# Performance work log

Hardware: AMD Instinct MI355X
Metric: run time of the kernel (lower is better)

The kernel has to match this reference:

```python
import jax, jax.numpy as jnp
import numpy as np

# Constants derived from init_kwargs (nuScenes occupancy setup)
XYZ_MIN = jnp.array([-40.0, -40.0, -1.0], dtype=jnp.float32)
XYZ_MAX = jnp.array([40.0, 40.0, 5.4], dtype=jnp.float32)
STEPSIZE = 0.5
_ext = np.array([80.0, 80.0, 6.4])
VOXEL_SIZE = float((_ext.prod() / (200 * 200 * 16)) ** (1.0 / 3.0))  # = 0.4
N_SAMPLES = int(np.linalg.norm(np.array([100, 100, 8]) + 1) / STEPSIZE) + 1  # 287


def trilinear_sample(grid, pts):
    """grid: (C, Dx, Dy, Dz) laid out as [C, x, y, z]; pts: (M, 3) world xyz -> (M, C).
    Matches torch F.grid_sample(align_corners=True) after the coord flip in grid_sampler:
    normalized coord u in [0,1] maps to index u*(dim-1)."""
    C, Dx, Dy, Dz = grid.shape
    dims = jnp.array([Dx, Dy, Dz], dtype=pts.dtype)
    u = (pts - XYZ_MIN) / (XYZ_MAX - XYZ_MIN)
    idx = jnp.clip(u * (dims - 1.0), 0.0, dims - 1.0)  # out-of-bbox pts are masked later
    i0 = jnp.clip(jnp.floor(idx), 0.0, dims - 2.0).astype(jnp.int32)
    w = idx - i0  # (M, 3) in [0, 1]
    flat = grid.reshape(C, -1)
    out = jnp.zeros((C, pts.shape[0]), dtype=pts.dtype)
    for ox in (0, 1):
        wx = w[:, 0] if ox else 1.0 - w[:, 0]
        for oy in (0, 1):
            wy = w[:, 1] if oy else 1.0 - w[:, 1]
            for oz in (0, 1):
                wz = w[:, 2] if oz else 1.0 - w[:, 2]
                lin = ((i0[:, 0] + ox) * Dy + (i0[:, 1] + oy)) * Dz + (i0[:, 2] + oz)
                out = out + jnp.take(flat, lin, axis=1) * (wx * wy * wz)
    return out.T


def _forward(rays_o, rays_d, voxel, rgb_recon):
    ro = rays_o.reshape(-1, 3)
    rd = rays_d.reshape(-1, 3)
    R = ro.shape[0]
    # test-mode sampling: rng = arange(N_samples), Zval = stepsize * voxel_size * rng
    zval = (STEPSIZE * VOXEL_SIZE) * jnp.arange(N_SAMPLES, dtype=ro.dtype)  # (N,)
    pts = ro[:, None, :] + rd[:, None, :] * zval[None, :, None]  # (R, N, 3)
    inside = jnp.all((pts >= XYZ_MIN) & (pts <= XYZ_MAX), axis=-1)  # ~mask_outbbox, (R, N)
    flat_pts = pts.reshape(-1, 3)
    # density sigmoid -> 'prob' compositing
    dens = trilinear_sample(voxel, flat_pts).reshape(R, N_SAMPLES)
    sig = jax.nn.sigmoid(dens)
    # probs = 0 outside bbox; last sample forced to 1 unless inside (then overwritten by sig)
    probs = jnp.where(inside, sig, 0.0)
    probs = probs.at[:, -1].set(jnp.where(inside[:, -1], sig[:, -1], 1.0))
    cum = jnp.minimum(jnp.cumsum(probs, axis=1), 1.0)  # cumsum.clamp(max=1)
    probs = jnp.diff(cum, axis=1, prepend=jnp.zeros((R, 1), cum.dtype))
    depth = jnp.sum(probs * zval[None, :], axis=-1)  # (R,)
    # rgb rendering (img_recon_head=True)
    rgb = trilinear_sample(rgb_recon, flat_pts).reshape(R, N_SAMPLES, 3)
    rgb = jnp.where(inside[..., None], rgb, 0.0)
    rgb_marched = jnp.sum(probs[..., None] * rgb, axis=-2)  # (R, 3)
    return depth, rgb_marched


def setup_inputs() -> dict:
    key = jax.random.key(0)
    k1, k2, k3, k4 = jax.random.split(key, 4)
    num_cam, H, W = 6, 90, 160
    # camera origins near the scene center, inside the bbox
    rays_o = (jax.random.uniform(k1, (num_cam, H, W, 3), jnp.float32) - 0.5) \
        * jnp.array([4.0, 4.0, 1.0], jnp.float32) + jnp.array([0.0, 0.0, 1.5], jnp.float32)
    d = jax.random.normal(k2, (num_cam, H, W, 3), jnp.float32)
    rays_d = d / jnp.linalg.norm(d, axis=-1, keepdims=True)
    voxel = jax.random.normal(k3, (1, 200, 200, 16), jnp.float32)
    rgb_recon = jax.random.uniform(k4, (3, 200, 200, 16), jnp.float32)
    return {"rays_o": rays_o, "rays_d": rays_d, "voxel": voxel, "rgb_recon": rgb_recon}


def reference(rays_o, rays_d, voxel, rgb_recon):
    return _forward(rays_o, rays_d, voxel, rgb_recon)
```

## Files before the change

kernel.cpp:

```cpp
#include <hip/hip_runtime.h>
#include <hip/hip_bf16.h>


namespace {
constexpr int DX = 200, DY = 200, DZ = 16;
constexpr int GRID_N = DX * DY * DZ;
constexpr int NS = 287;
constexpr float ZSTEP = 0.2f;
}

extern "C" __global__ void __launch_bounds__(256)
nerf_march_kernel(const float* __restrict__ ro,
                  const float* __restrict__ rd,
                  const float* __restrict__ vox,
                  const float* __restrict__ rgbg,
                  float* __restrict__ out, int R)
{
    const int r = blockIdx.x * blockDim.x + threadIdx.x;
    if (r >= R) return;

    const float ox = ro[3 * r + 0];
    const float oy = ro[3 * r + 1];
    const float oz = ro[3 * r + 2];
    const float dx = rd[3 * r + 0];
    const float dy = rd[3 * r + 1];
    const float dz = rd[3 * r + 2];

    float c = 0.0f;
    float depth = 0.0f;
    float a0 = 0.0f, a1 = 0.0f, a2 = 0.0f;
    const float zlast = ZSTEP * (float)(NS - 1);

    #pragma unroll 1
    for (int n = 0; n < NS; ++n) {
        const float z  = ZSTEP * (float)n;
        const float px = ox + dx * z;
        const float py = oy + dy * z;
        const float pz = oz + dz * z;

        const bool inside = (px >= -40.0f) & (px <= 40.0f) &
                            (py >= -40.0f) & (py <= 40.0f) &
                            (pz >= -1.0f)  & (pz <= 5.4f);
        if (!inside) {
            if (c < 1.0f) depth += (1.0f - c) * zlast;
            break;
        }

        float fx = fminf(fmaxf((px + 40.0f) / 80.0f * 199.0f, 0.0f), 199.0f);
        float fy = fminf(fmaxf((py + 40.0f) / 80.0f * 199.0f, 0.0f), 199.0f);
        float fz = fminf(fmaxf((pz + 1.0f)  / 6.4f  * 15.0f,  0.0f), 15.0f);
        int ix = min((int)fx, DX - 2);
        int iy = min((int)fy, DY - 2);
        int iz = min((int)fz, DZ - 2);
        const float wx = fx - (float)ix, wy = fy - (float)iy, wz = fz - (float)iz;
        const float ux = 1.0f - wx, uy = 1.0f - wy, uz = 1.0f - wz;

        const float w000 = ux * uy * uz, w001 = ux * uy * wz;
        const float w010 = ux * wy * uz, w011 = ux * wy * wz;
        const float w100 = wx * uy * uz, w101 = wx * uy * wz;
        const float w110 = wx * wy * uz, w111 = wx * wy * wz;

        const int base = (ix * DY + iy) * DZ + iz;
        const int SX = DY * DZ;
        const int SY = DZ;

        const float dens =
            vox[base]           * w000 + vox[base + 1]           * w001 +
            vox[base + SY]      * w010 + vox[base + SY + 1]      * w011 +
            vox[base + SX]      * w100 + vox[base + SX + 1]      * w101 +
            vox[base + SX + SY] * w110 + vox[base + SX + SY + 1] * w111;

        const float sig = 1.0f / (1.0f + __expf(-dens));

        const float newc = c + sig;
        const float p = fminf(newc, 1.0f) - fminf(c, 1.0f);

        depth += p * z;

        #pragma unroll
        for (int ch = 0; ch < 3; ++ch) {
            const float* g = rgbg + ch * GRID_N;
            const float v =
                g[base]           * w000 + g[base + 1]           * w001 +
                g[base + SY]      * w010 + g[base + SY + 1]      * w011 +
                g[base + SX]      * w100 + g[base + SX + 1]      * w101 +
                g[base + SX + SY] * w110 + g[base + SX + SY + 1] * w111;
            if (ch == 0) a0 += p * v;
            else if (ch == 1) a1 += p * v;
            else a2 += p * v;
        }

        c = newc;
        if (c >= 1.0f) break;
    }

    out[r]             = depth;
    out[R + 3 * r]     = a0;
    out[R + 3 * r + 1] = a1;
    out[R + 3 * r + 2] = a2;
}

extern "C" void kernel_launch(void* const* d_in, const int* in_sizes, int n_in,
                              void* d_out, int out_size, void* d_ws, size_t ws_size,
                              hipStream_t stream) {
    const float* ro   = (const float*)d_in[0];
    const float* rd   = (const float*)d_in[1];
    const float* vox  = (const float*)d_in[2];
    const float* rgbg = (const float*)d_in[3];
    float* out = (float*)d_out;

    const int R = in_sizes[0] / 3;
    const int block = 256;
    const int grid = (R + block - 1) / block;

    nerf_march_kernel<<<grid, block, 0, stream>>>(ro, rd, vox, rgbg, out, R);
}
```

Before: 71.75 us.

## Pack density and RGB grids into interleaved float4 volume for single-load trilinear gathers

Adds a pre-pass kernel that interleaves the density grid and the three RGB channel grids into one float4 array in workspace. The march kernel then reads each of the 8 trilinear corners with one 16-byte load instead of four scattered scalar loads. Block size drops to 64 and the normalisation arithmetic is folded into FMAs. The trade-off is an extra kernel that reads and writes about 10MB per call, which adds launch cost and memory traffic on every invocation.

```diff
diff --git a/kernel.cpp b/kernel.cpp
--- a/kernel.cpp
+++ b/kernel.cpp
@@ -1,5 +1,4 @@
 #include <hip/hip_runtime.h>
-#include <hip/hip_bf16.h>
 
 
 namespace {
@@ -10,13 +9,27 @@
 }
 
 extern "C" __global__ void __launch_bounds__(256)
+nerf_pack_kernel(const float* __restrict__ vox,
+                 const float* __restrict__ rgbg,
+                 float4* __restrict__ pack)
+{
+    const int i = blockIdx.x * 256 + threadIdx.x;
+    if (i >= GRID_N) return;
+    float4 v;
+    v.x = vox[i];
+    v.y = rgbg[i];
+    v.z = rgbg[GRID_N + i];
+    v.w = rgbg[2 * GRID_N + i];
+    pack[i] = v;
+}
+
+extern "C" __global__ void __launch_bounds__(64)
 nerf_march_kernel(const float* __restrict__ ro,
                   const float* __restrict__ rd,
-                  const float* __restrict__ vox,
-                  const float* __restrict__ rgbg,
+                  const float4* __restrict__ pack,
                   float* __restrict__ out, int R)
 {
-    const int r = blockIdx.x * blockDim.x + threadIdx.x;
+    const int r = blockIdx.x * 64 + threadIdx.x;
     if (r >= R) return;
 
     const float ox = ro[3 * r + 0];
@@ -34,9 +47,9 @@
     #pragma unroll 1
     for (int n = 0; n < NS; ++n) {
         const float z  = ZSTEP * (float)n;
-        const float px = ox + dx * z;
-        const float py = oy + dy * z;
-        const float pz = oz + dz * z;
+        const float px = fmaf(dx, z, ox);
+        const float py = fmaf(dy, z, oy);
+        const float pz = fmaf(dz, z, oz);
 
         const bool inside = (px >= -40.0f) & (px <= 40.0f) &
                             (py >= -40.0f) & (py <= 40.0f) &
@@ -46,12 +59,12 @@
             break;
         }
 
-        float fx = fminf(fmaxf((px + 40.0f) / 80.0f * 199.0f, 0.0f), 199.0f);
-        float fy = fminf(fmaxf((py + 40.0f) / 80.0f * 199.0f, 0.0f), 199.0f);
-        float fz = fminf(fmaxf((pz + 1.0f)  / 6.4f  * 15.0f,  0.0f), 15.0f);
-        int ix = min((int)fx, DX - 2);
-        int iy = min((int)fy, DY - 2);
-        int iz = min((int)fz, DZ - 2);
+        const float fx = fminf(fmaxf(fmaf(px, 2.4875f,  99.5f),    0.0f), 199.0f);
+        const float fy = fminf(fmaxf(fmaf(py, 2.4875f,  99.5f),    0.0f), 199.0f);
+        const float fz = fminf(fmaxf(fmaf(pz, 2.34375f, 2.34375f), 0.0f), 15.0f);
+        const int ix = min((int)fx, DX - 2);
+        const int iy = min((int)fy, DY - 2);
+        const int iz = min((int)fz, DZ - 2);
         const float wx = fx - (float)ix, wy = fy - (float)iy, wz = fz - (float)iz;
         const float ux = 1.0f - wx, uy = 1.0f - wy, uz = 1.0f - wz;
 
@@ -61,34 +74,41 @@
         const float w110 = wx * wy * uz, w111 = wx * wy * wz;
 
         const int base = (ix * DY + iy) * DZ + iz;
-        const int SX = DY * DZ;
-        const int SY = DZ;
+        constexpr int SX = DY * DZ;
+        constexpr int SY = DZ;
+
+        const float4 c000 = pack[base];
+        const float4 c001 = pack[base + 1];
+        const float4 c010 = pack[base + SY];
+        const float4 c011 = pack[base + SY + 1];
+        const float4 c100 = pack[base + SX];
+        const float4 c101 = pack[base + SX + 1];
+        const float4 c110 = pack[base + SX + SY];
+        const float4 c111 = pack[base + SX + SY + 1];
 
         const float dens =
-            vox[base]           * w000 + vox[base + 1]           * w001 +
-            vox[base + SY]      * w010 + vox[base + SY + 1]      * w011 +
-            vox[base + SX]      * w100 + vox[base + SX + 1]      * w101 +
-            vox[base + SX + SY] * w110 + vox[base + SX + SY + 1] * w111;
+            c000.x * w000 + c001.x * w001 + c010.x * w010 + c011.x * w011 +
+            c100.x * w100 + c101.x * w101 + c110.x * w110 + c111.x * w111;
 
         const float sig = 1.0f / (1.0f + __expf(-dens));
 
         const float newc = c + sig;
-        const float p = fminf(newc, 1.0f) - fminf(c, 1.0f);
+        const float p = fminf(newc, 1.0f) - c;
 
         depth += p * z;
 
-        #pragma unroll
-        for (int ch = 0; ch < 3; ++ch) {
-            const float* g = rgbg + ch * GRID_N;
-            const float v =
-                g[base]           * w000 + g[base + 1]           * w001 +
-                g[base + SY]      * w010 + g[base + SY + 1]      * w011 +
-                g[base + SX]      * w100 + g[base + SX + 1]      * w101 +
-                g[base + SX + SY] * w110 + g[base + SX + SY + 1] * w111;
-            if (ch == 0) a0 += p * v;
-            else if (ch == 1) a1 += p * v;
-            else a2 += p * v;
-        }
+        const float vr =
+            c000.y * w000 + c001.y * w001 + c010.y * w010 + c011.y * w011 +
+            c100.y * w100 + c101.y * w101 + c110.y * w110 + c111.y * w111;
+        const float vg =
+            c000.z * w000 + c001.z * w001 + c010.z * w010 + c011.z * w011 +
+            c100.z * w100 + c101.z * w101 + c110.z * w110 + c111.z * w111;
+        const float vb =
+            c000.w * w000 + c001.w * w001 + c010.w * w010 + c011.w * w011 +
+            c100.w * w100 + c101.w * w101 + c110.w * w110 + c111.w * w111;
+        a0 += p * vr;
+        a1 += p * vg;
+        a2 += p * vb;
 
         c = newc;
         if (c >= 1.0f) break;
@@ -107,11 +127,11 @@
     const float* rd   = (const float*)d_in[1];
     const float* vox  = (const float*)d_in[2];
     const float* rgbg = (const float*)d_in[3];
+    float4* pack = (float4*)d_ws;
     float* out = (float*)d_out;
 
     const int R = in_sizes[0] / 3;
-    const int block = 256;
-    const int grid = (R + block - 1) / block;
 
-    nerf_march_kernel<<<grid, block, 0, stream>>>(ro, rd, vox, rgbg, out, R);
+    nerf_pack_kernel<<<(GRID_N + 255) / 256, 256, 0, stream>>>(vox, rgbg, pack);
+    nerf_march_kernel<<<(R + 63) / 64, 64, 0, stream>>>(ro, rd, pack, out, R);
 }
```

Measured after the change: 74.87 us. +4.3%, slower.

## Process ray samples in unrolled chunks of four with wave-uniform early exit

Applied to the files above, without the earlier changes.

The per-sample march loop becomes chunks of four unrolled, branchless samples. Out-of-box samples are masked to zero contribution instead of breaking, and termination is checked once per chunk with a wave-wide vote. This lets the compiler issue the trilinear gathers for several samples together, which raises memory-level parallelism and removes per-sample divergent branches. The cost is up to three wasted samples per ray and extra register pressure. The grid normalisation is also folded into single FMAs.

```diff
diff --git a/kernel.cpp b/kernel.cpp
--- a/kernel.cpp
+++ b/kernel.cpp
@@ -1,5 +1,4 @@
 #include <hip/hip_runtime.h>
-#include <hip/hip_bf16.h>
 
 
 namespace {
@@ -7,6 +6,7 @@
 constexpr int GRID_N = DX * DY * DZ;
 constexpr int NS = 287;
 constexpr float ZSTEP = 0.2f;
+constexpr int CH = 4;
 }
 
 extern "C" __global__ void __launch_bounds__(256)
@@ -29,70 +29,76 @@
     float c = 0.0f;
     float depth = 0.0f;
     float a0 = 0.0f, a1 = 0.0f, a2 = 0.0f;
+    bool  exited = false;
     const float zlast = ZSTEP * (float)(NS - 1);
 
     #pragma unroll 1
-    for (int n = 0; n < NS; ++n) {
-        const float z  = ZSTEP * (float)n;
-        const float px = ox + dx * z;
-        const float py = oy + dy * z;
-        const float pz = oz + dz * z;
+    for (int n0 = 0; n0 < NS; n0 += CH) {
+        #pragma unroll
+        for (int j = 0; j < CH; ++j) {
+            const int   n = n0 + j;
+            const float z = ZSTEP * (float)n;
+            const float px = fmaf(dx, z, ox);
+            const float py = fmaf(dy, z, oy);
+            const float pz = fmaf(dz, z, oz);
 
-        const bool inside = (px >= -40.0f) & (px <= 40.0f) &
-                            (py >= -40.0f) & (py <= 40.0f) &
-                            (pz >= -1.0f)  & (pz <= 5.4f);
-        if (!inside) {
-            if (c < 1.0f) depth += (1.0f - c) * zlast;
-            break;
+            const bool real   = (n < NS);
+            const bool in_box = (px >= -40.0f) & (px <= 40.0f) &
+                                (py >= -40.0f) & (py <= 40.0f) &
+                                (pz >= -1.0f)  & (pz <= 5.4f);
+            const bool valid  = real & in_box;
+            exited |= (real & !in_box);
+
+            const float fx = fminf(fmaxf(fmaf(px, 2.4875f,  99.5f),    0.0f), 199.0f);
+            const float fy = fminf(fmaxf(fmaf(py, 2.4875f,  99.5f),    0.0f), 199.0f);
+            const float fz = fminf(fmaxf(fmaf(pz, 2.34375f, 2.34375f), 0.0f), 15.0f);
+            const int ix = min((int)fx, DX - 2);
+            const int iy = min((int)fy, DY - 2);
+            const int iz = min((int)fz, DZ - 2);
+            const float wx = fx - (float)ix, wy = fy - (float)iy, wz = fz - (float)iz;
+            const float ux = 1.0f - wx, uy = 1.0f - wy, uz = 1.0f - wz;
+
+            const float w000 = ux * uy * uz, w001 = ux * uy * wz;
+            const float w010 = ux * wy * uz, w011 = ux * wy * wz;
+            const float w100 = wx * uy * uz, w101 = wx * uy * wz;
+            const float w110 = wx * wy * uz, w111 = wx * wy * wz;
+
+            const int base = (ix * DY + iy) * DZ + iz;
+            constexpr int SX = DY * DZ;
+            constexpr int SY = DZ;
+
+            const float dens =
+                vox[base]           * w000 + vox[base + 1]           * w001 +
+                vox[base + SY]      * w010 + vox[base + SY + 1]      * w011 +
+                vox[base + SX]      * w100 + vox[base + SX + 1]      * w101 +
+                vox[base + SX + SY] * w110 + vox[base + SX + SY + 1] * w111;
+
+            const float sig = valid ? (1.0f / (1.0f + __expf(-dens))) : 0.0f;
+
+            const float newc = c + sig;
+            const float p = fminf(newc, 1.0f) - fminf(c, 1.0f);
+
+            depth = fmaf(p, z, depth);
+
+            #pragma unroll
+            for (int ch = 0; ch < 3; ++ch) {
+                const float* g = rgbg + ch * GRID_N;
+                const float v =
+                    g[base]           * w000 + g[base + 1]           * w001 +
+                    g[base + SY]      * w010 + g[base + SY + 1]      * w011 +
+                    g[base + SX]      * w100 + g[base + SX + 1]      * w101 +
+                    g[base + SX + SY] * w110 + g[base + SX + SY + 1] * w111;
+                if      (ch == 0) a0 = fmaf(p, v, a0);
+                else if (ch == 1) a1 = fmaf(p, v, a1);
+                else              a2 = fmaf(p, v, a2);
+            }
+
+            c = newc;
         }
+        if (__all((c >= 1.0f) || exited)) break;
+    }
 
-        float fx = fminf(fmaxf((px + 40.0f) / 80.0f * 199.0f, 0.0f), 199.0f);
-        float fy = fminf(fmaxf((py + 40.0f) / 80.0f * 199.0f, 0.0f), 199.0f);
-        float fz = fminf(fmaxf((pz + 1.0f)  / 6.4f  * 15.0f,  0.0f), 15.0f);
-        int ix = min((int)fx, DX - 2);
-        int iy = min((int)fy, DY - 2);
-        int iz = min((int)fz, DZ - 2);
-        const float wx = fx - (float)ix, wy = fy - (float)iy, wz = fz - (float)iz;
-        const float ux = 1.0f - wx, uy = 1.0f - wy, uz = 1.0f - wz;
-
-        const float w000 = ux * uy * uz, w001 = ux * uy * wz;
-        const float w010 = ux * wy * uz, w011 = ux * wy * wz;
-        const float w100 = wx * uy * uz, w101 = wx * uy * wz;
-        const float w110 = wx * wy * uz, w111 = wx * wy * wz;
-
-        const int base = (ix * DY + iy) * DZ + iz;
-        const int SX = DY * DZ;
-        const int SY = DZ;
-
-        const float dens =
-            vox[base]           * w000 + vox[base + 1]           * w001 +
-            vox[base + SY]      * w010 + vox[base + SY + 1]      * w011 +
-            vox[base + SX]      * w100 + vox[base + SX + 1]      * w101 +
-            vox[base + SX + SY] * w110 + vox[base + SX + SY + 1] * w111;
-
-        const float sig = 1.0f / (1.0f + __expf(-dens));
-
-        const float newc = c + sig;
-        const float p = fminf(newc, 1.0f) - fminf(c, 1.0f);
-
-        depth += p * z;
-
-        #pragma unroll
-        for (int ch = 0; ch < 3; ++ch) {
-            const float* g = rgbg + ch * GRID_N;
-            const float v =
-                g[base]           * w000 + g[base + 1]           * w001 +
-                g[base + SY]      * w010 + g[base + SY + 1]      * w011 +
-                g[base + SX]      * w100 + g[base + SX + 1]      * w101 +
-                g[base + SX + SY] * w110 + g[base + SX + SY + 1] * w111;
-            if (ch == 0) a0 += p * v;
-            else if (ch == 1) a1 += p * v;
-            else a2 += p * v;
-        }
-
-        c = newc;
-        if (c >= 1.0f) break;
-    }
+    if (exited && (c < 1.0f)) depth = fmaf(1.0f - c, zlast, depth);
 
     out[r]             = depth;
     out[R + 3 * r]     = a0;
```

New measurement: 77.78 us. +8.4%, slower.
